# Kernel optimization log

Measured on AMD Instinct MI355X. Metric: run time of the kernel, lower is better.

The kernel has to match this reference:

```python
import jax, jax.numpy as jnp
import numpy as np

B, T, OBS = 16, 256, 128
W0 = 256          # widths = [256, 256], num_hidden = 1
HID = 256         # rnn_hidden_dim
CTX = 64
A = 64            # action_dim
RANK = 4
HN_H = 128        # hypernet hidden
DELTA_SCALE = 0.05
LV_MIN, LV_MAX = -6.0, 4.0


def setup_inputs() -> dict:
    key = jax.random.key(0)
    ks = jax.random.split(key, 32)
    s = 0.05
    def w(k, shape):
        return jax.random.normal(k, shape, dtype=jnp.float32) * s
    HN_OUT = HID * RANK + RANK * A + A  # 1344
    return {
        "obs_seq": jax.random.normal(ks[0], (B, T, OBS), dtype=jnp.float32),
        "h0": jnp.zeros((1, B, HID), dtype=jnp.float32),
        # encoder MLP (torch Linear convention: W is [out, in])
        "W_in": w(ks[1], (W0, OBS)),   "b_in": w(ks[2], (W0,)),
        "W_h1": w(ks[3], (W0, W0)),    "b_h1": w(ks[4], (W0,)),
        # GRU (gate order r, z, n as in torch)
        "gru_Wih": w(ks[5], (3 * HID, W0)),  "gru_Whh": w(ks[6], (3 * HID, HID)),
        "gru_bih": w(ks[7], (3 * HID,)),     "gru_bhh": w(ks[8], (3 * HID,)),
        # context heads
        "W_mu": w(ks[9], (CTX, HID)),  "b_mu": w(ks[10], (CTX,)),
        "W_lv": w(ks[11], (CTX, HID)), "b_lv": w(ks[12], (CTX,)),
        # scalar gate params
        "gate_w": jnp.float32(1.0), "gate_b": jnp.float32(0.0),
        # base policy head
        "W_pol": w(ks[13], (A, HID)), "b_pol": w(ks[14], (A,)),
        # hypernet MLP: ctx -> 128 -> 128 -> HN_OUT
        "hn_W1": w(ks[15], (HN_H, CTX)),  "hn_b1": w(ks[16], (HN_H,)),
        "hn_W2": w(ks[17], (HN_H, HN_H)), "hn_b2": w(ks[18], (HN_H,)),
        "hn_W3": w(ks[19], (HN_OUT, HN_H)), "hn_b3": w(ks[20], (HN_OUT,)),
    }


def _gru(x_seq, h0, Wih, Whh, bih, bhh):
    """Batch-first GRU. x_seq: [B,T,D], h0: [B,H] -> (feats [B,T,H], hT [B,H])."""
    # precompute input-side gate pre-activations: [T, B, 3H]
    xg = jnp.einsum("btd,gd->tbg", x_seq, Wih) + bih

    def step(h, xg_t):
        hg = h @ Whh.T + bhh                       # [B, 3H]
        xr, xz, xn = jnp.split(xg_t, 3, axis=-1)
        hr, hz, hn = jnp.split(hg, 3, axis=-1)
        r = jax.nn.sigmoid(xr + hr)
        z = jax.nn.sigmoid(xz + hz)
        n = jnp.tanh(xn + r * hn)
        h_new = (1.0 - z) * n + z * h
        return h_new, h_new

    hT, feats = jax.lax.scan(step, h0, xg)
    return jnp.transpose(feats, (1, 0, 2)), hT      # [B,T,H], [B,H]


def reference(obs_seq, h0, W_in, b_in, W_h1, b_h1,
              gru_Wih, gru_Whh, gru_bih, gru_bhh,
              W_mu, b_mu, W_lv, b_lv, gate_w, gate_b,
              W_pol, b_pol, hn_W1, hn_b1, hn_W2, hn_b2, hn_W3, hn_b3):
    # ---- encoder MLP ----
    x = jax.nn.relu(obs_seq @ W_in.T + b_in)
    x = jax.nn.relu(x @ W_h1.T + b_h1)             # [B,T,W0]

    # ---- GRU ----
    feats, hT = _gru(x, h0[0], gru_Wih, gru_Whh, gru_bih, gru_bhh)  # [B,T,H]
    hn_state = hT[None]                            # [1,B,H]

    # ---- context heads + uncertainty gate ----
    ctx_mu = feats @ W_mu.T + b_mu                 # [B,T,CTX]
    ctx_lv = jnp.clip(feats @ W_lv.T + b_lv, LV_MIN, LV_MAX)
    mean_lv = jnp.mean(ctx_lv, axis=-1, keepdims=True)      # [B,T,1]
    gate = jax.nn.sigmoid(gate_w * (-mean_lv) + gate_b)     # [B,T,1]

    # ---- low-rank hypernet deltas ----
    h1 = jax.nn.relu(ctx_mu @ hn_W1.T + hn_b1)
    h2 = jax.nn.relu(h1 @ hn_W2.T + hn_b2)
    deltas = (h2 @ hn_W3.T + hn_b3) * DELTA_SCALE  # [B,T,H*r + r*A + A]
    w_end = HID * RANK
    a_end = w_end + RANK * A
    Bn, Tn = obs_seq.shape[0], obs_seq.shape[1]
    wf = deltas[..., :w_end].reshape(Bn, Tn, HID, RANK)     # [B,T,H,r]
    af = deltas[..., w_end:a_end].reshape(Bn, Tn, RANK, A)  # [B,T,r,A]
    db = deltas[..., a_end:]                                # [B,T,A]

    delta_w = jnp.einsum("bthr,btra->btha", wf, af)         # [B,T,H,A] (large)
    base_w = W_pol.T[None, None]                            # [1,1,H,A]
    eff_w = base_w + gate[..., None] * delta_w
    eff_b = b_pol[None, None] + gate * db
    logits = jnp.einsum("bth,btha->bta", feats, eff_w) + eff_b
    return logits, hn_state
```

## Files before the change

kernel.cpp:

```cpp
#include <hip/hip_runtime.h>
#include <cstddef>

#define BB 16
#define TT 256
#define OBSD 128
#define W0D 256
#define HID 256
#define CTX 64
#define NA 64
#define HNH 128
#define HNOUT 1344
#define MROWS 4096

__device__ __forceinline__ float sigm(float x) { return 1.f / (1.f + __expf(-x)); }
__device__ __forceinline__ float tanh_f(float x) { return 1.f - 2.f / (__expf(2.f * x) + 1.f); }

__global__ __launch_bounds__(256) void gemm_bt(
    const float* __restrict__ A, const float* __restrict__ Bw,
    const float* __restrict__ bias, float* __restrict__ C,
    int M, int N, int K, int act, float scale)
{
    __shared__ float As[16][132];
    __shared__ float Bs[16][68];
    const int tid = threadIdx.x;
    const int m0 = blockIdx.x * 128, n0 = blockIdx.y * 64;
    const int tx = tid & 15, ty = tid >> 4;
    float acc[8][4] = {};
    for (int k0 = 0; k0 < K; k0 += 16) {
#pragma unroll
        for (int l = 0; l < 2; ++l) {
            int v = tid + l * 256;
            int row = v >> 2, kc = (v & 3) << 2;
            float4 a4 = *(const float4*)(A + (size_t)(m0 + row) * K + k0 + kc);
            As[kc + 0][row] = a4.x; As[kc + 1][row] = a4.y;
            As[kc + 2][row] = a4.z; As[kc + 3][row] = a4.w;
        }
        {
            int row = tid >> 2, kc = (tid & 3) << 2;
            float4 b4 = *(const float4*)(Bw + (size_t)(n0 + row) * K + k0 + kc);
            Bs[kc + 0][row] = b4.x; Bs[kc + 1][row] = b4.y;
            Bs[kc + 2][row] = b4.z; Bs[kc + 3][row] = b4.w;
        }
        __syncthreads();
#pragma unroll
        for (int k = 0; k < 16; ++k) {
            float4 a0 = *(const float4*)&As[k][ty * 8];
            float4 a1 = *(const float4*)&As[k][ty * 8 + 4];
            float4 b0 = *(const float4*)&Bs[k][tx * 4];
            float a[8] = {a0.x, a0.y, a0.z, a0.w, a1.x, a1.y, a1.z, a1.w};
            float b[4] = {b0.x, b0.y, b0.z, b0.w};
#pragma unroll
            for (int i = 0; i < 8; ++i)
#pragma unroll
                for (int jj = 0; jj < 4; ++jj)
                    acc[i][jj] = fmaf(a[i], b[jj], acc[i][jj]);
        }
        __syncthreads();
    }
    const float4 bia = *(const float4*)(bias + n0 + tx * 4);
    const float bb[4] = {bia.x, bia.y, bia.z, bia.w};
#pragma unroll
    for (int i = 0; i < 8; ++i) {
        int m = m0 + ty * 8 + i;
        float4 o;
        float* op = &o.x;
#pragma unroll
        for (int jj = 0; jj < 4; ++jj) {
            float v = acc[i][jj] + bb[jj];
            if (act) v = fmaxf(v, 0.f);
            op[jj] = v * scale;
        }
        *(float4*)(C + (size_t)m * N + n0 + tx * 4) = o;
    }
}

typedef _Float16 f16x8 __attribute__((ext_vector_type(8)));
typedef float f32x4 __attribute__((ext_vector_type(4)));

__global__ __launch_bounds__(512, 2) void gru_mfma_kernel(
    const float* __restrict__ XG, const float* __restrict__ Whh,
    const float* __restrict__ bhh, const float* __restrict__ h0,
    float* __restrict__ FE, float* __restrict__ HT)
{
    __shared__ __align__(16) _Float16 hbuf[2][256];
    const int b = blockIdx.x;
    const int tid = threadIdx.x;
    const int wv = tid >> 6;
    const int l  = tid & 63;
    const int c  = l & 15;
    const int q  = l >> 4;

    f16x8 wreg[6][8];
#pragma unroll
    for (int ti = 0; ti < 6; ++ti) {
        const int g = ti >> 1;
        const int j = 32 * wv + (ti & 1) * 16 + c;
        const float* row = Whh + (size_t)(g * 256 + j) * 256 + q * 8;
#pragma unroll
        for (int ks = 0; ks < 8; ++ks) {
            float4 f0 = *(const float4*)(row + ks * 32);
            float4 f1 = *(const float4*)(row + ks * 32 + 4);
            f16x8 v;
            v[0] = (_Float16)f0.x; v[1] = (_Float16)f0.y;
            v[2] = (_Float16)f0.z; v[3] = (_Float16)f0.w;
            v[4] = (_Float16)f1.x; v[5] = (_Float16)f1.y;
            v[6] = (_Float16)f1.z; v[7] = (_Float16)f1.w;
            wreg[ti][ks] = v;
        }
    }
    const int j1 = 32 * wv + c, j2 = j1 + 16;
    const float br1 = bhh[j1], bz1 = bhh[256 + j1], bn1 = bhh[512 + j1];
    const float br2 = bhh[j2], bz2 = bhh[256 + j2], bn2 = bhh[512 + j2];
    float h1o = 0.f, h2o = 0.f;
    if (l < 16) {
        h1o = h0[b * 256 + j1]; h2o = h0[b * 256 + j2];
        hbuf[0][j1] = (_Float16)h1o; hbuf[0][j2] = (_Float16)h2o;
    }
    __syncthreads();
    const float* xgp = XG + (size_t)b * TT * 768;
    float* fep = FE + (size_t)b * TT * HID;
    for (int t = 0; t < TT; ++t) {
        float xr1, xz1, xn1, xr2, xz2, xn2;
        if (l < 16) {
            xr1 = xgp[j1]; xz1 = xgp[256 + j1]; xn1 = xgp[512 + j1];
            xr2 = xgp[j2]; xz2 = xgp[256 + j2]; xn2 = xgp[512 + j2];
        }
        f32x4 a0 = {0.f, 0.f, 0.f, 0.f}, a1 = a0, a2 = a0,
              a3 = a0, a4 = a0, a5 = a0;
        const _Float16* hb = hbuf[t & 1] + q * 8;
#pragma unroll
        for (int ks = 0; ks < 8; ++ks) {
            f16x8 af = *(const f16x8*)(hb + ks * 32);
            a0 = __builtin_amdgcn_mfma_f32_16x16x32_f16(af, wreg[0][ks], a0, 0, 0, 0);
            a1 = __builtin_amdgcn_mfma_f32_16x16x32_f16(af, wreg[1][ks], a1, 0, 0, 0);
            a2 = __builtin_amdgcn_mfma_f32_16x16x32_f16(af, wreg[2][ks], a2, 0, 0, 0);
            a3 = __builtin_amdgcn_mfma_f32_16x16x32_f16(af, wreg[3][ks], a3, 0, 0, 0);
            a4 = __builtin_amdgcn_mfma_f32_16x16x32_f16(af, wreg[4][ks], a4, 0, 0, 0);
            a5 = __builtin_amdgcn_mfma_f32_16x16x32_f16(af, wreg[5][ks], a5, 0, 0, 0);
        }
        if (l < 16) {
            float r1 = sigm(xr1 + a0[0] + br1);
            float z1 = sigm(xz1 + a2[0] + bz1);
            float n1 = tanh_f(xn1 + r1 * (a4[0] + bn1));
            h1o = (1.f - z1) * n1 + z1 * h1o;
            float r2 = sigm(xr2 + a1[0] + br2);
            float z2 = sigm(xz2 + a3[0] + bz2);
            float n2 = tanh_f(xn2 + r2 * (a5[0] + bn2));
            h2o = (1.f - z2) * n2 + z2 * h2o;
            _Float16* nb = hbuf[(t + 1) & 1];
            nb[j1] = (_Float16)h1o; nb[j2] = (_Float16)h2o;
            fep[j1] = h1o; fep[j2] = h2o;
        }
        xgp += 768; fep += HID;
        __syncthreads();
    }
    if (l < 16) { HT[b * HID + j1] = h1o; HT[b * HID + j2] = h2o; }
}

__global__ __launch_bounds__(256) void mid_kernel(
    const float* __restrict__ FE,
    const float* __restrict__ W_mu, const float* __restrict__ b_mu,
    const float* __restrict__ W_lv, const float* __restrict__ b_lv,
    const float* __restrict__ gw_p, const float* __restrict__ gb_p,
    const float* __restrict__ W1, const float* __restrict__ b1,
    const float* __restrict__ W2, const float* __restrict__ b2,
    float* __restrict__ GATE, float* __restrict__ H2out)
{
    __shared__ float fT[256][20];
    __shared__ float muT[64][20];
    __shared__ float h1T[128][20];
    __shared__ float lvb[16][68];
    const int tid = threadIdx.x;
    const int r0 = blockIdx.x * 16;
#pragma unroll
    for (int l = 0; l < 4; ++l) {
        int v = tid + l * 256;
        int t = v >> 6, kc = (v & 63) << 2;
        float4 f = *(const float4*)(FE + (size_t)(r0 + t) * HID + kc);
        fT[kc + 0][t] = f.x; fT[kc + 1][t] = f.y;
        fT[kc + 2][t] = f.z; fT[kc + 3][t] = f.w;
    }
    __syncthreads();
    const int c = tid & 127, tg = tid >> 7;
    {
        const float* wrow = (c < 64) ? (W_mu + (size_t)c * HID)
                                     : (W_lv + (size_t)(c - 64) * HID);
        float acc[8] = {};
        for (int k = 0; k < 256; k += 4) {
            float4 wv = *(const float4*)(wrow + k);
#pragma unroll
            for (int e = 0; e < 4; ++e) {
                float wsc = (&wv.x)[e];
                float4 fa = *(const float4*)&fT[k + e][tg * 8];
                float4 fb = *(const float4*)&fT[k + e][tg * 8 + 4];
                acc[0] = fmaf(wsc, fa.x, acc[0]); acc[1] = fmaf(wsc, fa.y, acc[1]);
                acc[2] = fmaf(wsc, fa.z, acc[2]); acc[3] = fmaf(wsc, fa.w, acc[3]);
                acc[4] = fmaf(wsc, fb.x, acc[4]); acc[5] = fmaf(wsc, fb.y, acc[5]);
                acc[6] = fmaf(wsc, fb.z, acc[6]); acc[7] = fmaf(wsc, fb.w, acc[7]);
            }
        }
        float bb2 = (c < 64) ? b_mu[c] : b_lv[c - 64];
#pragma unroll
        for (int i2 = 0; i2 < 8; ++i2) {
            int t = tg * 8 + i2;
            float v = acc[i2] + bb2;
            if (c < 64) muT[c][t] = v;
            else        lvb[t][c - 64] = fminf(fmaxf(v, -6.f), 4.f);
        }
    }
    __syncthreads();
    if (tid < 16) {
        float s = 0.f;
        for (int i2 = 0; i2 < 64; ++i2) s += lvb[tid][i2];
        float mean = s * (1.f / 64.f);
        GATE[r0 + tid] = sigm(gw_p[0] * (-mean) + gb_p[0]);
    }
    {
        const float* wrow = W1 + (size_t)c * CTX;
        float acc[8] = {};
        for (int k = 0; k < 64; k += 4) {
            float4 wv = *(const float4*)(wrow + k);
#pragma unroll
            for (int e = 0; e < 4; ++e) {
                float wsc = (&wv.x)[e];
                float4 fa = *(const float4*)&muT[k + e][tg * 8];
                float4 fb = *(const float4*)&muT[k + e][tg * 8 + 4];
                acc[0] = fmaf(wsc, fa.x, acc[0]); acc[1] = fmaf(wsc, fa.y, acc[1]);
                acc[2] = fmaf(wsc, fa.z, acc[2]); acc[3] = fmaf(wsc, fa.w, acc[3]);
                acc[4] = fmaf(wsc, fb.x, acc[4]); acc[5] = fmaf(wsc, fb.y, acc[5]);
                acc[6] = fmaf(wsc, fb.z, acc[6]); acc[7] = fmaf(wsc, fb.w, acc[7]);
            }
        }
        float bb2 = b1[c];
#pragma unroll
        for (int i2 = 0; i2 < 8; ++i2) {
            int t = tg * 8 + i2;
            h1T[c][t] = fmaxf(acc[i2] + bb2, 0.f);
        }
    }
    __syncthreads();
    {
        const float* wrow = W2 + (size_t)c * HNH;
        float acc[8] = {};
        for (int k = 0; k < 128; k += 4) {
            float4 wv = *(const float4*)(wrow + k);
#pragma unroll
            for (int e = 0; e < 4; ++e) {
                float wsc = (&wv.x)[e];
                float4 fa = *(const float4*)&h1T[k + e][tg * 8];
                float4 fb = *(const float4*)&h1T[k + e][tg * 8 + 4];
                acc[0] = fmaf(wsc, fa.x, acc[0]); acc[1] = fmaf(wsc, fa.y, acc[1]);
                acc[2] = fmaf(wsc, fa.z, acc[2]); acc[3] = fmaf(wsc, fa.w, acc[3]);
                acc[4] = fmaf(wsc, fb.x, acc[4]); acc[5] = fmaf(wsc, fb.y, acc[5]);
                acc[6] = fmaf(wsc, fb.z, acc[6]); acc[7] = fmaf(wsc, fb.w, acc[7]);
            }
        }
        float bb2 = b2[c];
#pragma unroll
        for (int i2 = 0; i2 < 8; ++i2) {
            int t = tg * 8 + i2;
            H2out[(size_t)(r0 + t) * HNH + c] = fmaxf(acc[i2] + bb2, 0.f);
        }
    }
}

__global__ __launch_bounds__(256) void final_kernel(
    const float* __restrict__ FE, const float* __restrict__ DL,
    const float* __restrict__ GATE, const float* __restrict__ W_pol,
    const float* __restrict__ b_pol, float* __restrict__ OUT)
{
    __shared__ float fs[4][256];
    __shared__ float dsb[4][HNOUT];
    __shared__ float sr[4][4];
    __shared__ float gg[4];
    const int tid = threadIdx.x;
    const int r0 = blockIdx.x * 4;
    {
        int t = tid >> 6, kc = (tid & 63) << 2;
        *(float4*)&fs[t][kc] = *(const float4*)(FE + (size_t)(r0 + t) * HID + kc);
    }
    for (int v = tid; v < 1344; v += 256) {
        int t = v / 336, qq = v - t * 336;
        ((float4*)&dsb[t][0])[qq] = ((const float4*)(DL + (size_t)(r0 + t) * HNOUT))[qq];
    }
    if (tid < 4) gg[tid] = GATE[r0 + tid];
    __syncthreads();
    {
        const int t = tid >> 6, lane = tid & 63;
        float p0 = 0, p1 = 0, p2 = 0, p3 = 0;
#pragma unroll
        for (int hh = 0; hh < 4; ++hh) {
            int h = lane + hh * 64;
            float f = fs[t][h];
            float4 d4 = *(const float4*)&dsb[t][4 * h];
            p0 = fmaf(f, d4.x, p0); p1 = fmaf(f, d4.y, p1);
            p2 = fmaf(f, d4.z, p2); p3 = fmaf(f, d4.w, p3);
        }
#pragma unroll
        for (int off = 32; off >= 1; off >>= 1) {
            p0 += __shfl_down(p0, off);
            p1 += __shfl_down(p1, off);
            p2 += __shfl_down(p2, off);
            p3 += __shfl_down(p3, off);
        }
        if (lane == 0) { sr[t][0] = p0; sr[t][1] = p1; sr[t][2] = p2; sr[t][3] = p3; }
    }
    __syncthreads();
    {
        const int t = tid >> 6, a = tid & 63;
        const float* wrow = W_pol + (size_t)a * HID;
        float acc = 0.f;
        for (int k = 0; k < 256; k += 4) {
            float4 wv = *(const float4*)(wrow + k);
            float4 fv = *(const float4*)&fs[t][k];
            acc = fmaf(wv.x, fv.x, acc); acc = fmaf(wv.y, fv.y, acc);
            acc = fmaf(wv.z, fv.z, acc); acc = fmaf(wv.w, fv.w, acc);
        }
        float la = sr[t][0] * dsb[t][1024 + a] + sr[t][1] * dsb[t][1088 + a]
                 + sr[t][2] * dsb[t][1152 + a] + sr[t][3] * dsb[t][1216 + a]
                 + dsb[t][1280 + a];
        OUT[(size_t)(r0 + t) * NA + a] = acc + b_pol[a] + gg[t] * la;
    }
}

extern "C" void kernel_launch(void* const* d_in, const int* in_sizes, int n_in,
                              void* d_out, int out_size, void* d_ws, size_t ws_size,
                              hipStream_t stream) {
    const float* obs   = (const float*)d_in[0];
    const float* h0    = (const float*)d_in[1];
    const float* W_in  = (const float*)d_in[2];
    const float* b_in  = (const float*)d_in[3];
    const float* W_h1  = (const float*)d_in[4];
    const float* b_h1  = (const float*)d_in[5];
    const float* Wih   = (const float*)d_in[6];
    const float* Whh   = (const float*)d_in[7];
    const float* bih   = (const float*)d_in[8];
    const float* bhh   = (const float*)d_in[9];
    const float* W_mu  = (const float*)d_in[10];
    const float* b_mu  = (const float*)d_in[11];
    const float* W_lv  = (const float*)d_in[12];
    const float* b_lv  = (const float*)d_in[13];
    const float* gate_w= (const float*)d_in[14];
    const float* gate_b= (const float*)d_in[15];
    const float* W_pol = (const float*)d_in[16];
    const float* b_pol = (const float*)d_in[17];
    const float* hn_W1 = (const float*)d_in[18];
    const float* hn_b1 = (const float*)d_in[19];
    const float* hn_W2 = (const float*)d_in[20];
    const float* hn_b2 = (const float*)d_in[21];
    const float* hn_W3 = (const float*)d_in[22];
    const float* hn_b3 = (const float*)d_in[23];

    float* ws = (float*)d_ws;
    float* X1 = ws;
    float* X2 = X1 + 1048576;
    float* XG = X2 + 1048576;
    float* FE = XG + 3145728;
    float* GA = FE + 1048576;
    float* H2 = GA + 4096;
    float* DL = H2 + 524288;
    (void)ws_size; (void)n_in; (void)in_sizes; (void)out_size;

    float* logits = (float*)d_out;
    float* hn_out = logits + (size_t)BB * TT * NA;

    gemm_bt<<<dim3(32, 4), 256, 0, stream>>>(obs, W_in, b_in, X1, MROWS, 256, 128, 1, 1.f);
    gemm_bt<<<dim3(32, 4), 256, 0, stream>>>(X1, W_h1, b_h1, X2, MROWS, 256, 256, 1, 1.f);
    gemm_bt<<<dim3(32, 12), 256, 0, stream>>>(X2, Wih, bih, XG, MROWS, 768, 256, 0, 1.f);
    gru_mfma_kernel<<<16, 512, 0, stream>>>(XG, Whh, bhh, h0, FE, hn_out);
    mid_kernel<<<256, 256, 0, stream>>>(FE, W_mu, b_mu, W_lv, b_lv, gate_w, gate_b,
                                        hn_W1, hn_b1, hn_W2, hn_b2, GA, H2);
    gemm_bt<<<dim3(32, 21), 256, 0, stream>>>(H2, hn_W3, hn_b3, DL, MROWS, HNOUT, 128, 0, 0.05f);
    final_kernel<<<1024, 256, 0, stream>>>(FE, DL, GA, W_pol, b_pol, logits);
}
```

Baseline: 585.3 us.

## Prefetch GRU input gates into LDS in 8-step chunks with async loads

The GRU recurrence kernel now streams the precomputed input-gate activations for 8 timesteps at a time into a double-buffered shared-memory region using global-to-LDS async loads, prefetching the next chunk while the current one is consumed. Per-step synchronisation is replaced with a barrier that waits only on LDS counters, with a full memory wait once per chunk. This aims to take global-load latency off the serial per-step critical path. It adds 48KB of shared memory per block, which may limit occupancy, and relies on hand-written waitcnt semantics.

```diff
diff --git a/kernel.cpp b/kernel.cpp
--- a/kernel.cpp
+++ b/kernel.cpp
@@ -14,6 +14,13 @@
 
 __device__ __forceinline__ float sigm(float x) { return 1.f / (1.f + __expf(-x)); }
 __device__ __forceinline__ float tanh_f(float x) { return 1.f - 2.f / (__expf(2.f * x) + 1.f); }
+
+#define LDS_BARRIER() asm volatile("s_waitcnt lgkmcnt(0)\n\ts_barrier" ::: "memory")
+#define FULL_BARRIER() asm volatile("s_waitcnt vmcnt(0) lgkmcnt(0)\n\ts_barrier" ::: "memory")
+#define GLOAD_LDS16(g, l)                                                      \
+    __builtin_amdgcn_global_load_lds(                                          \
+        (const __attribute__((address_space(1))) void*)(g),                    \
+        (__attribute__((address_space(3))) void*)(l), 16, 0, 0)
 
 __global__ __launch_bounds__(256) void gemm_bt(
     const float* __restrict__ A, const float* __restrict__ Bw,
@@ -82,6 +89,7 @@
     const float* __restrict__ bhh, const float* __restrict__ h0,
     float* __restrict__ FE, float* __restrict__ HT)
 {
+    __shared__ __align__(16) float xgbuf[2][8 * 768];
     __shared__ __align__(16) _Float16 hbuf[2][256];
     const int b = blockIdx.x;
     const int tid = threadIdx.x;
@@ -116,43 +124,64 @@
         h1o = h0[b * 256 + j1]; h2o = h0[b * 256 + j2];
         hbuf[0][j1] = (_Float16)h1o; hbuf[0][j2] = (_Float16)h2o;
     }
-    __syncthreads();
-    const float* xgp = XG + (size_t)b * TT * 768;
-    float* fep = FE + (size_t)b * TT * HID;
-    for (int t = 0; t < TT; ++t) {
-        float xr1, xz1, xn1, xr2, xz2, xn2;
-        if (l < 16) {
-            xr1 = xgp[j1]; xz1 = xgp[256 + j1]; xn1 = xgp[512 + j1];
-            xr2 = xgp[j2]; xz2 = xgp[256 + j2]; xn2 = xgp[512 + j2];
-        }
-        f32x4 a0 = {0.f, 0.f, 0.f, 0.f}, a1 = a0, a2 = a0,
-              a3 = a0, a4 = a0, a5 = a0;
-        const _Float16* hb = hbuf[t & 1] + q * 8;
-#pragma unroll
-        for (int ks = 0; ks < 8; ++ks) {
-            f16x8 af = *(const f16x8*)(hb + ks * 32);
-            a0 = __builtin_amdgcn_mfma_f32_16x16x32_f16(af, wreg[0][ks], a0, 0, 0, 0);
-            a1 = __builtin_amdgcn_mfma_f32_16x16x32_f16(af, wreg[1][ks], a1, 0, 0, 0);
-            a2 = __builtin_amdgcn_mfma_f32_16x16x32_f16(af, wreg[2][ks], a2, 0, 0, 0);
-            a3 = __builtin_amdgcn_mfma_f32_16x16x32_f16(af, wreg[3][ks], a3, 0, 0, 0);
-            a4 = __builtin_amdgcn_mfma_f32_16x16x32_f16(af, wreg[4][ks], a4, 0, 0, 0);
-            a5 = __builtin_amdgcn_mfma_f32_16x16x32_f16(af, wreg[5][ks], a5, 0, 0, 0);
-        }
-        if (l < 16) {
-            float r1 = sigm(xr1 + a0[0] + br1);
-            float z1 = sigm(xz1 + a2[0] + bz1);
-            float n1 = tanh_f(xn1 + r1 * (a4[0] + bn1));
-            h1o = (1.f - z1) * n1 + z1 * h1o;
-            float r2 = sigm(xr2 + a1[0] + br2);
-            float z2 = sigm(xz2 + a3[0] + bz2);
-            float n2 = tanh_f(xn2 + r2 * (a5[0] + bn2));
-            h2o = (1.f - z2) * n2 + z2 * h2o;
-            _Float16* nb = hbuf[(t + 1) & 1];
-            nb[j1] = (_Float16)h1o; nb[j2] = (_Float16)h2o;
-            fep[j1] = h1o; fep[j2] = h2o;
-        }
-        xgp += 768; fep += HID;
-        __syncthreads();
+    const float* xgbase = XG + (size_t)b * TT * 768;
+    float* feb = FE + (size_t)b * TT * HID;
+    {
+        const float* g = xgbase + wv * 768 + l * 4;
+        float* lb = &xgbuf[0][wv * 768];
+#pragma unroll
+        for (int i = 0; i < 3; ++i)
+            GLOAD_LDS16(g + i * 256, lb + i * 256);
+    }
+    FULL_BARRIER();
+    for (int ck = 0; ck < 32; ++ck) {
+        if (ck < 31) {
+            const float* g = xgbase + (size_t)(ck + 1) * 6144 + wv * 768 + l * 4;
+            float* lb = &xgbuf[(ck + 1) & 1][wv * 768];
+#pragma unroll
+            for (int i = 0; i < 3; ++i)
+                GLOAD_LDS16(g + i * 256, lb + i * 256);
+        }
+        const float* xc = &xgbuf[ck & 1][0];
+#pragma unroll
+        for (int s = 0; s < 8; ++s) {
+            const int t = ck * 8 + s;
+            float xr1, xz1, xn1, xr2, xz2, xn2;
+            if (l < 16) {
+                const float* p = xc + s * 768;
+                xr1 = p[j1]; xz1 = p[256 + j1]; xn1 = p[512 + j1];
+                xr2 = p[j2]; xz2 = p[256 + j2]; xn2 = p[512 + j2];
+            }
+            f32x4 a0 = {0.f, 0.f, 0.f, 0.f}, a1 = a0, a2 = a0,
+                  a3 = a0, a4 = a0, a5 = a0;
+            const _Float16* hb = hbuf[t & 1] + q * 8;
+#pragma unroll
+            for (int ks = 0; ks < 8; ++ks) {
+                f16x8 af = *(const f16x8*)(hb + ks * 32);
+                a0 = __builtin_amdgcn_mfma_f32_16x16x32_f16(af, wreg[0][ks], a0, 0, 0, 0);
+                a1 = __builtin_amdgcn_mfma_f32_16x16x32_f16(af, wreg[1][ks], a1, 0, 0, 0);
+                a2 = __builtin_amdgcn_mfma_f32_16x16x32_f16(af, wreg[2][ks], a2, 0, 0, 0);
+                a3 = __builtin_amdgcn_mfma_f32_16x16x32_f16(af, wreg[3][ks], a3, 0, 0, 0);
+                a4 = __builtin_amdgcn_mfma_f32_16x16x32_f16(af, wreg[4][ks], a4, 0, 0, 0);
+                a5 = __builtin_amdgcn_mfma_f32_16x16x32_f16(af, wreg[5][ks], a5, 0, 0, 0);
+            }
+            if (l < 16) {
+                float r1 = sigm(xr1 + a0[0] + br1);
+                float z1 = sigm(xz1 + a2[0] + bz1);
+                float n1 = tanh_f(xn1 + r1 * (a4[0] + bn1));
+                h1o = (1.f - z1) * n1 + z1 * h1o;
+                float r2 = sigm(xr2 + a1[0] + br2);
+                float z2 = sigm(xz2 + a3[0] + bz2);
+                float n2 = tanh_f(xn2 + r2 * (a5[0] + bn2));
+                h2o = (1.f - z2) * n2 + z2 * h2o;
+                _Float16* nb = hbuf[(t + 1) & 1];
+                nb[j1] = (_Float16)h1o; nb[j2] = (_Float16)h2o;
+                float* fp = feb + (size_t)t * HID;
+                fp[j1] = h1o; fp[j2] = h2o;
+            }
+            if (s < 7) LDS_BARRIER();
+        }
+        FULL_BARRIER();
     }
     if (l < 16) { HT[b * HID + j1] = h1o; HT[b * HID + j2] = h2o; }
 }
```

After: 591.7 us. No clear change (+1.1%).
